# Kernel optimization log

Hardware: AMD Instinct MI355X
Metric: run time of the kernel (lower is better)

The kernel has to match this reference:

```python
import jax, jax.numpy as jnp
import numpy as np

DIM = 1024
N_HEADS = 16
HEAD_DIM = DIM // N_HEADS


def setup_inputs() -> dict:
    key = jax.random.key(0)
    ks = jax.random.split(key, 5)
    B, L = 2, 2048
    q = jax.random.normal(ks[0], (B, L, DIM), dtype=jnp.float32)
    # nn.Linear weights: shape [out_features, in_features], applied as x @ W.T
    scale = 1.0 / np.sqrt(DIM)
    Wq = jax.random.normal(ks[1], (DIM, DIM), dtype=jnp.float32) * scale
    Wk = jax.random.normal(ks[2], (DIM, DIM), dtype=jnp.float32) * scale
    Wv = jax.random.normal(ks[3], (DIM, DIM), dtype=jnp.float32) * scale
    Wo = jax.random.normal(ks[4], (DIM, DIM), dtype=jnp.float32) * scale
    return {"q": q, "Wq": Wq, "Wk": Wk, "Wv": Wv, "Wo": Wo}


def reference(q, Wq, Wk, Wv, Wo):
    B, L, _ = q.shape
    kv = q  # self-attention (kv=None path)
    # projections: x @ W.T, then split heads: b l (h d) -> b h l d
    def split_heads(x):
        return x.reshape(B, L, N_HEADS, HEAD_DIM).transpose(0, 2, 1, 3)
    qh = split_heads(q @ Wq.T)
    kh = split_heads(kv @ Wk.T)
    vh = split_heads(kv @ Wv.T)
    # scaled dot-product attention; scale = sqrt(head_dim)
    scores = jnp.einsum('bhid,bhjd->bhij', qh, kh) / jnp.sqrt(
        jnp.asarray(HEAD_DIM, dtype=qh.dtype))
    attn = jax.nn.softmax(scores, axis=-1)
    out = jnp.einsum('bhij,bhjd->bhid', attn, vh)
    # b h l d -> b l (h d)
    out = out.transpose(0, 2, 1, 3).reshape(B, L, DIM)
    return out @ Wo.T
```

## Files before the change

### kernel.cpp

```cpp
#include <hip/hip_runtime.h>


#define DIMN 1024
#define NH 16
#define HD 64
#define BB 2
#define LL 2048

typedef float f32x4 __attribute__((ext_vector_type(4)));
typedef short s16x8 __attribute__((ext_vector_type(8)));

#define QSCALE 0.18033688011112042f

static __device__ __forceinline__ unsigned short f2bf(float f) {
  unsigned u = __float_as_uint(f);
  u += 0x7fffu + ((u >> 16) & 1u);
  return (unsigned short)(u >> 16);
}
static __device__ __forceinline__ unsigned packbf2(float lo, float hi) {
  return (unsigned)f2bf(lo) | ((unsigned)f2bf(hi) << 16);
}
static __device__ __forceinline__ float xexp2(float x) {
#if __has_builtin(__builtin_amdgcn_exp2f)
  return __builtin_amdgcn_exp2f(x);
#else
  return exp2f(x);
#endif
}
static __device__ __forceinline__ s16x8 cvt8(float4 a, float4 b) {
  s16x8 r;
  r[0] = (short)f2bf(a.x); r[1] = (short)f2bf(a.y);
  r[2] = (short)f2bf(a.z); r[3] = (short)f2bf(a.w);
  r[4] = (short)f2bf(b.x); r[5] = (short)f2bf(b.y);
  r[6] = (short)f2bf(b.z); r[7] = (short)f2bf(b.w);
  return r;
}
static __device__ __forceinline__ void gld16(const unsigned short* g,
                                             unsigned short* l) {
#if __has_builtin(__builtin_amdgcn_global_load_lds)
  __builtin_amdgcn_global_load_lds(
      (const __attribute__((address_space(1))) void*)g,
      (__attribute__((address_space(3))) void*)l, 16, 0, 0);
#else
  ((uint4*)l)[threadIdx.x & 63] = ((const uint4*)g)[0];
#endif
}

__global__ __launch_bounds__(256) void cvt_all(
    const float* __restrict__ X, const float* __restrict__ Wq,
    const float* __restrict__ Wk, const float* __restrict__ Wv,
    const float* __restrict__ Wo, unsigned short* __restrict__ out) {
  const int seg = blockIdx.y;
  const float* src;
  unsigned short* dst;
  size_t n;
  if (seg == 0) { src = X; dst = out; n = (size_t)1 << 22; }
  else {
    src = (seg == 1) ? Wq : (seg == 2) ? Wk : (seg == 3) ? Wv : Wo;
    dst = out + ((size_t)1 << 22) + (size_t)(seg - 1) * (1u << 20);
    n = (size_t)1 << 20;
  }
  size_t i = ((size_t)blockIdx.x * 256 + threadIdx.x) * 8;
  if (i >= n) return;
  float4 v0 = *(const float4*)(src + i);
  float4 v1 = *(const float4*)(src + i + 4);
  uint4 o;
  o.x = packbf2(v0.x, v0.y); o.y = packbf2(v0.z, v0.w);
  o.z = packbf2(v1.x, v1.y); o.w = packbf2(v1.z, v1.w);
  *(uint4*)(dst + i) = o;
}

__global__ __launch_bounds__(256) void gemm_qkv(
    const unsigned short* __restrict__ Xb, const unsigned short* __restrict__ Wb,
    unsigned short* __restrict__ Qb, unsigned short* __restrict__ Kb,
    unsigned short* __restrict__ VT) {
  __shared__ __align__(16) unsigned short Al[128 * 32];
  __shared__ __align__(16) unsigned short Bl[128 * 32];
  const int m0 = blockIdx.x * 128;
  const int n0g = blockIdx.y * 128;
  const int sel = n0g >> 10;
  const int tid = threadIdx.x;
  const int w = tid >> 6, lane = tid & 63;
  const int c = lane & 15, quad = lane >> 4;
  const int wm = (w & 1) * 64, wn = (w >> 1) * 64;

  f32x4 zero = {0.f, 0.f, 0.f, 0.f};
  f32x4 acc[4][4];
#pragma unroll
  for (int i = 0; i < 4; ++i)
#pragma unroll
    for (int j = 0; j < 4; ++j) acc[i][j] = zero;

  const int srow = w * 32 + (lane >> 2);
  const int scol = (lane & 3) * 8;
  const unsigned short* gA = Xb + (size_t)(m0 + srow) * DIMN + scol;
  const unsigned short* gB = Wb + (size_t)(n0g + srow) * DIMN + scol;
  unsigned short* lA0 = Al + (w * 32) * 32;
  unsigned short* lA1 = Al + (w * 32 + 16) * 32;
  unsigned short* lB0 = Bl + (w * 32) * 32;
  unsigned short* lB1 = Bl + (w * 32 + 16) * 32;

  for (int k0 = 0; k0 < DIMN; k0 += 32) {
    __syncthreads();
    gld16(gA + k0, lA0);
    gld16(gA + k0 + 16 * DIMN, lA1);
    gld16(gB + k0, lB0);
    gld16(gB + k0 + 16 * DIMN, lB1);
    __syncthreads();
    s16x8 a[4], b[4];
#pragma unroll
    for (int i = 0; i < 4; ++i)
      a[i] = *(const s16x8*)&Al[(wm + i * 16 + c) * 32 + quad * 8];
#pragma unroll
    for (int j = 0; j < 4; ++j)
      b[j] = *(const s16x8*)&Bl[(wn + j * 16 + c) * 32 + quad * 8];
    if (sel != 2) {
#pragma unroll
      for (int i = 0; i < 4; ++i)
#pragma unroll
        for (int j = 0; j < 4; ++j)
          acc[i][j] = __builtin_amdgcn_mfma_f32_16x16x32_bf16(a[i], b[j], acc[i][j], 0, 0, 0);
    } else {
#pragma unroll
      for (int i = 0; i < 4; ++i)
#pragma unroll
        for (int j = 0; j < 4; ++j)
          acc[i][j] = __builtin_amdgcn_mfma_f32_16x16x32_bf16(b[j], a[i], acc[i][j], 0, 0, 0);
    }
  }

  const int n0 = n0g & 1023;
  if (sel != 2) {
    unsigned short* Out = (sel == 0) ? Qb : Kb;
    const float scale = (sel == 0) ? QSCALE : 1.0f;
#pragma unroll
    for (int i = 0; i < 4; ++i)
#pragma unroll
      for (int j = 0; j < 4; ++j)
#pragma unroll
        for (int r = 0; r < 4; ++r) {
          int row = m0 + wm + i * 16 + quad * 4 + r;
          int col = n0 + wn + j * 16 + c;
          Out[(((size_t)(row >> 11) * NH + (col >> 6)) * LL + (row & 2047)) * HD + (col & 63)] =
              f2bf(acc[i][j][r] * scale);
        }
  } else {
#pragma unroll
    for (int i = 0; i < 4; ++i)
#pragma unroll
      for (int j = 0; j < 4; ++j)
#pragma unroll
        for (int r = 0; r < 4; ++r) {
          int n = n0 + wn + j * 16 + quad * 4 + r;
          int m = m0 + wm + i * 16 + c;
          VT[(((size_t)(m >> 11) * NH + (n >> 6)) * HD + (n & 63)) * LL + (m & 2047)] =
              f2bf(acc[i][j][r]);
        }
  }
}

__global__ __launch_bounds__(256) void gemm_o(
    const unsigned short* __restrict__ A, const unsigned short* __restrict__ Wob,
    float* __restrict__ Out) {
  __shared__ __align__(16) unsigned short Al[128 * 32];
  __shared__ __align__(16) unsigned short Bl[128 * 32];
  const int m0 = blockIdx.x * 128;
  const int n0 = blockIdx.y * 128;
  const int tid = threadIdx.x;
  const int w = tid >> 6, lane = tid & 63;
  const int c = lane & 15, quad = lane >> 4;
  const int wm = (w & 1) * 64, wn = (w >> 1) * 64;

  f32x4 zero = {0.f, 0.f, 0.f, 0.f};
  f32x4 acc[4][4];
#pragma unroll
  for (int i = 0; i < 4; ++i)
#pragma unroll
    for (int j = 0; j < 4; ++j) acc[i][j] = zero;

  const int srow = w * 32 + (lane >> 2);
  const int scol = (lane & 3) * 8;
  const unsigned short* gA = A + (size_t)(m0 + srow) * DIMN + scol;
  const unsigned short* gB = Wob + (size_t)(n0 + srow) * DIMN + scol;
  unsigned short* lA0 = Al + (w * 32) * 32;
  unsigned short* lA1 = Al + (w * 32 + 16) * 32;
  unsigned short* lB0 = Bl + (w * 32) * 32;
  unsigned short* lB1 = Bl + (w * 32 + 16) * 32;

  for (int k0 = 0; k0 < DIMN; k0 += 32) {
    __syncthreads();
    gld16(gA + k0, lA0);
    gld16(gA + k0 + 16 * DIMN, lA1);
    gld16(gB + k0, lB0);
    gld16(gB + k0 + 16 * DIMN, lB1);
    __syncthreads();
    s16x8 a[4], b[4];
#pragma unroll
    for (int i = 0; i < 4; ++i)
      a[i] = *(const s16x8*)&Al[(wm + i * 16 + c) * 32 + quad * 8];
#pragma unroll
    for (int j = 0; j < 4; ++j)
      b[j] = *(const s16x8*)&Bl[(wn + j * 16 + c) * 32 + quad * 8];
#pragma unroll
    for (int i = 0; i < 4; ++i)
#pragma unroll
      for (int j = 0; j < 4; ++j)
        acc[i][j] = __builtin_amdgcn_mfma_f32_16x16x32_bf16(a[i], b[j], acc[i][j], 0, 0, 0);
  }

#pragma unroll
  for (int i = 0; i < 4; ++i)
#pragma unroll
    for (int j = 0; j < 4; ++j)
#pragma unroll
      for (int r = 0; r < 4; ++r)
        Out[(size_t)(m0 + wm + i * 16 + quad * 4 + r) * DIMN + n0 + wn + j * 16 + c] =
            acc[i][j][r];
}

__global__ __launch_bounds__(64) void qkv_proj_f(
    const float* __restrict__ X, const float* __restrict__ Wq,
    const float* __restrict__ Wk, const float* __restrict__ Wv,
    unsigned short* __restrict__ Qb, unsigned short* __restrict__ Kb,
    unsigned short* __restrict__ VT) {
  const int m0 = blockIdx.x * 64;
  const int n0g = blockIdx.y * 64;
  const int sel = n0g >> 10;
  const int n0 = n0g & 1023;
  const float* W = (sel == 0) ? Wq : (sel == 1) ? Wk : Wv;
  const int lane = threadIdx.x;
  const int c = lane & 15, quad = lane >> 4;

  f32x4 zero = {0.f, 0.f, 0.f, 0.f};
  f32x4 acc[4][4];
#pragma unroll
  for (int i = 0; i < 4; ++i)
#pragma unroll
    for (int j = 0; j < 4; ++j) acc[i][j] = zero;

  const float* ab = X + (size_t)(m0 + c) * DIMN + quad * 8;
  const float* bb = W + (size_t)(n0 + c) * DIMN + quad * 8;

  for (int k0 = 0; k0 < DIMN; k0 += 32) {
    s16x8 a[4], b[4];
#pragma unroll
    for (int i = 0; i < 4; ++i) {
      const float* p = ab + i * 16 * DIMN + k0;
      a[i] = cvt8(*(const float4*)p, *(const float4*)(p + 4));
    }
#pragma unroll
    for (int j = 0; j < 4; ++j) {
      const float* p = bb + j * 16 * DIMN + k0;
      b[j] = cvt8(*(const float4*)p, *(const float4*)(p + 4));
    }
    if (sel != 2) {
#pragma unroll
      for (int i = 0; i < 4; ++i)
#pragma unroll
        for (int j = 0; j < 4; ++j)
          acc[i][j] = __builtin_amdgcn_mfma_f32_16x16x32_bf16(a[i], b[j], acc[i][j], 0, 0, 0);
    } else {
#pragma unroll
      for (int i = 0; i < 4; ++i)
#pragma unroll
        for (int j = 0; j < 4; ++j)
          acc[i][j] = __builtin_amdgcn_mfma_f32_16x16x32_bf16(b[j], a[i], acc[i][j], 0, 0, 0);
    }
  }

  if (sel != 2) {
    unsigned short* Out = (sel == 0) ? Qb : Kb;
    const float scale = (sel == 0) ? QSCALE : 1.0f;
#pragma unroll
    for (int i = 0; i < 4; ++i)
#pragma unroll
      for (int j = 0; j < 4; ++j)
#pragma unroll
        for (int r = 0; r < 4; ++r) {
          int row = m0 + i * 16 + quad * 4 + r;
          int nl = n0 + j * 16 + c;
          int bi = row >> 11, li = row & 2047;
          int h = nl >> 6, d = nl & 63;
          Out[(((size_t)bi * NH + h) * LL + li) * HD + d] = f2bf(acc[i][j][r] * scale);
        }
  } else {
#pragma unroll
    for (int i = 0; i < 4; ++i)
#pragma unroll
      for (int j = 0; j < 4; ++j)
#pragma unroll
        for (int r = 0; r < 4; ++r) {
          int n = n0 + j * 16 + quad * 4 + r;
          int l = m0 + i * 16 + c;
          int h = n >> 6, d = n & 63;
          int bi = l >> 11, li = l & 2047;
          VT[(((size_t)bi * NH + h) * HD + d) * LL + li] = f2bf(acc[i][j][r]);
        }
  }
}

__global__ __launch_bounds__(256) void attn2(
    const unsigned short* __restrict__ Qb, const unsigned short* __restrict__ Kb,
    const unsigned short* __restrict__ VT, unsigned short* __restrict__ AO) {
  __shared__ __align__(16) unsigned short Kl[64][72];
  __shared__ __align__(16) unsigned short Vtl[64][72];
  __shared__ __align__(16) unsigned short Pl[4][16][72];

  const int bh = blockIdx.y;
  const int tid = threadIdx.x;
  const int w = tid >> 6, lane = tid & 63;
  const int c = lane & 15, quad = lane >> 4;
  const int q0 = blockIdx.x * 64 + w * 16;

  const unsigned short* Qh = Qb + (size_t)bh * LL * HD;
  const unsigned short* Kh = Kb + (size_t)bh * LL * HD;
  const unsigned short* Vh = VT + (size_t)bh * HD * LL;

  s16x8 qf0 = *(const s16x8*)(Qh + (size_t)(q0 + c) * HD + quad * 8);
  s16x8 qf1 = *(const s16x8*)(Qh + (size_t)(q0 + c) * HD + 32 + quad * 8);

  f32x4 zero = {0.f, 0.f, 0.f, 0.f};
  f32x4 o[4];
  float lsum[4] = {0.f, 0.f, 0.f, 0.f};
#pragma unroll
  for (int dc = 0; dc < 4; ++dc) o[dc] = zero;

  const int krow = tid >> 2, kq = tid & 3;
  const int vd = tid >> 2, vh = (tid >> 1) & 1, vc0 = (tid & 1) * 8;

  for (int k0 = 0; k0 < LL; k0 += 64) {
    __syncthreads();
    {
      const unsigned short* ks = Kh + (size_t)(k0 + krow) * HD + kq * 16;
      uint4 ka = *(const uint4*)ks;
      uint4 kb2 = *(const uint4*)(ks + 8);
      const unsigned short* vs = Vh + (size_t)vd * LL + k0 + vh * 32 + vc0;
      uint4 va = *(const uint4*)vs;
      uint4 vb = *(const uint4*)(vs + 16);
      *(uint4*)&Kl[krow][kq * 16] = ka;
      *(uint4*)&Kl[krow][kq * 16 + 8] = kb2;
      const unsigned* ap = (const unsigned*)&va;
      const unsigned* bp = (const unsigned*)&vb;
      unsigned ov[8];
#pragma unroll
      for (int j = 0; j < 4; ++j) {
        ov[2 * j]     = __builtin_amdgcn_perm(bp[j], ap[j], 0x05040100u);
        ov[2 * j + 1] = __builtin_amdgcn_perm(bp[j], ap[j], 0x07060302u);
      }
      uint4 w0 = {ov[0], ov[1], ov[2], ov[3]};
      uint4 w1 = {ov[4], ov[5], ov[6], ov[7]};
      *(uint4*)&Vtl[vd][vh * 32 + vc0 * 2] = w0;
      *(uint4*)&Vtl[vd][vh * 32 + vc0 * 2 + 8] = w1;
    }
    __syncthreads();

    f32x4 s[4];
#pragma unroll
    for (int t = 0; t < 4; ++t) {
      s16x8 kfa = *(const s16x8*)&Kl[t * 16 + c][quad * 8];
      s16x8 kfb = *(const s16x8*)&Kl[t * 16 + c][32 + quad * 8];
      s[t] = __builtin_amdgcn_mfma_f32_16x16x32_bf16(qf0, kfa, zero, 0, 0, 0);
      s[t] = __builtin_amdgcn_mfma_f32_16x16x32_bf16(qf1, kfb, s[t], 0, 0, 0);
    }

#pragma unroll
    for (int r = 0; r < 4; ++r) {
      float p0 = xexp2(s[0][r]);
      float p1 = xexp2(s[1][r]);
      float p2 = xexp2(s[2][r]);
      float p3 = xexp2(s[3][r]);
      lsum[r] += (p0 + p1) + (p2 + p3);
      unsigned pk01 = __builtin_amdgcn_perm(__float_as_uint(p1), __float_as_uint(p0), 0x07060302u);
      unsigned pk23 = __builtin_amdgcn_perm(__float_as_uint(p3), __float_as_uint(p2), 0x07060302u);
      int row = quad * 4 + r;
      *(unsigned*)&Pl[w][row][2 * c] = pk01;
      *(unsigned*)&Pl[w][row][32 + 2 * c] = pk23;
    }
    asm volatile("s_waitcnt lgkmcnt(0)" ::: "memory");

#pragma unroll
    for (int kk = 0; kk < 2; ++kk) {
      s16x8 pf = *(const s16x8*)&Pl[w][c][kk * 32 + quad * 8];
#pragma unroll
      for (int dc = 0; dc < 4; ++dc) {
        s16x8 vf = *(const s16x8*)&Vtl[dc * 16 + c][kk * 32 + quad * 8];
        o[dc] = __builtin_amdgcn_mfma_f32_16x16x32_bf16(pf, vf, o[dc], 0, 0, 0);
      }
    }
  }

  const int bi = bh >> 4, h = bh & 15;
#pragma unroll
  for (int r = 0; r < 4; ++r) {
    float l = lsum[r];
    l += __shfl_xor(l, 1);
    l += __shfl_xor(l, 2);
    l += __shfl_xor(l, 4);
    l += __shfl_xor(l, 8);
    float inv = 1.0f / l;
    int li = q0 + quad * 4 + r;
#pragma unroll
    for (int dc = 0; dc < 4; ++dc)
      AO[((size_t)bi * LL + li) * DIMN + h * HD + dc * 16 + c] = f2bf(o[dc][r] * inv);
  }
}

__global__ __launch_bounds__(64) void o_proj_f(
    const unsigned short* __restrict__ A, const float* __restrict__ Wo,
    float* __restrict__ Out) {
  const int m0 = blockIdx.x * 64, n0 = blockIdx.y * 64;
  const int lane = threadIdx.x;
  const int c = lane & 15, quad = lane >> 4;

  f32x4 zero = {0.f, 0.f, 0.f, 0.f};
  f32x4 acc[4][4];
#pragma unroll
  for (int i = 0; i < 4; ++i)
#pragma unroll
    for (int j = 0; j < 4; ++j) acc[i][j] = zero;

  const unsigned short* ab = A + (size_t)(m0 + c) * DIMN + quad * 8;
  const float* bb = Wo + (size_t)(n0 + c) * DIMN + quad * 8;

  for (int k0 = 0; k0 < DIMN; k0 += 32) {
    s16x8 a[4], b[4];
#pragma unroll
    for (int i = 0; i < 4; ++i) a[i] = *(const s16x8*)(ab + i * 16 * DIMN + k0);
#pragma unroll
    for (int j = 0; j < 4; ++j) {
      const float* p = bb + j * 16 * DIMN + k0;
      b[j] = cvt8(*(const float4*)p, *(const float4*)(p + 4));
    }
#pragma unroll
    for (int i = 0; i < 4; ++i)
#pragma unroll
      for (int j = 0; j < 4; ++j)
        acc[i][j] = __builtin_amdgcn_mfma_f32_16x16x32_bf16(a[i], b[j], acc[i][j], 0, 0, 0);
  }

#pragma unroll
  for (int i = 0; i < 4; ++i)
#pragma unroll
    for (int j = 0; j < 4; ++j)
#pragma unroll
      for (int r = 0; r < 4; ++r)
        Out[(size_t)(m0 + i * 16 + quad * 4 + r) * DIMN + n0 + j * 16 + c] = acc[i][j][r];
}

extern "C" void kernel_launch(void* const* d_in, const int* in_sizes, int n_in,
                              void* d_out, int out_size, void* d_ws, size_t ws_size,
                              hipStream_t stream) {
  const float* X = (const float*)d_in[0];
  const float* Wq = (const float*)d_in[1];
  const float* Wk = (const float*)d_in[2];
  const float* Wv = (const float*)d_in[3];
  const float* Wo = (const float*)d_in[4];
  float* Out = (float*)d_out;

  const size_t M1 = (size_t)1 << 20;
  unsigned short* ws16 = (unsigned short*)d_ws;

  if (ws_size >= (size_t)48 * 1024 * 1024) {
    unsigned short* Xb = ws16;
    unsigned short* Wb = ws16 + 4 * M1;
    unsigned short* Qb = ws16 + 8 * M1;
    unsigned short* Kb = ws16 + 12 * M1;
    unsigned short* VT = ws16 + 16 * M1;
    unsigned short* AO = ws16 + 20 * M1;
    cvt_all<<<dim3(2048, 5), 256, 0, stream>>>(X, Wq, Wk, Wv, Wo, ws16);
    gemm_qkv<<<dim3(32, 24), 256, 0, stream>>>(Xb, Wb, Qb, Kb, VT);
    attn2<<<dim3(LL / 64, BB * NH), 256, 0, stream>>>(Qb, Kb, VT, AO);
    gemm_o<<<dim3(32, 8), 256, 0, stream>>>(AO, Wb + 3 * M1, Out);
  } else {
    unsigned short* Qb = ws16;
    unsigned short* Kb = ws16 + 4 * M1;
    unsigned short* VT = ws16 + 8 * M1;
    unsigned short* AO = ws16 + 12 * M1;
    qkv_proj_f<<<dim3(64, 48), 64, 0, stream>>>(X, Wq, Wk, Wv, Qb, Kb, VT);
    attn2<<<dim3(LL / 64, BB * NH), 256, 0, stream>>>(Qb, Kb, VT, AO);
    o_proj_f<<<dim3(64, 16), 64, 0, stream>>>(AO, Wo, Out);
  }
}
```

Before: 210.4 us.

## Double attention query tile per wave, narrow O-proj tile, flatten conversion grid

Each attention wave now processes 32 query rows, and a block covers 128 queries. This amortizes the K/V tile loads and shared-memory staging over twice the work, at the cost of more registers and fewer blocks. The output projection uses a 128x64 tile, doubling its grid to improve CU occupancy. The bf16 conversion kernel uses a dense 1D grid, so no blocks are launched only to exit early.

Measured after the change: 201.0 us. 4.5% less time.

```diff
diff --git a/kernel.cpp b/kernel.cpp
--- a/kernel.cpp
+++ b/kernel.cpp
@@ -50,18 +50,19 @@
     const float* __restrict__ X, const float* __restrict__ Wq,
     const float* __restrict__ Wk, const float* __restrict__ Wv,
     const float* __restrict__ Wo, unsigned short* __restrict__ out) {
-  const int seg = blockIdx.y;
+  const int blk = blockIdx.x;
   const float* src;
   unsigned short* dst;
-  size_t n;
-  if (seg == 0) { src = X; dst = out; n = (size_t)1 << 22; }
-  else {
-    src = (seg == 1) ? Wq : (seg == 2) ? Wk : (seg == 3) ? Wv : Wo;
-    dst = out + ((size_t)1 << 22) + (size_t)(seg - 1) * (1u << 20);
-    n = (size_t)1 << 20;
-  }
-  size_t i = ((size_t)blockIdx.x * 256 + threadIdx.x) * 8;
-  if (i >= n) return;
+  size_t off;
+  if (blk < 2048) {
+    src = X; dst = out; off = (size_t)blk * 2048;
+  } else {
+    int s = (blk - 2048) >> 9;
+    src = (s == 0) ? Wq : (s == 1) ? Wk : (s == 2) ? Wv : Wo;
+    dst = out + ((size_t)1 << 22) + (size_t)s * (1u << 20);
+    off = (size_t)((blk - 2048) & 511) * 2048;
+  }
+  size_t i = off + (size_t)threadIdx.x * 8;
   float4 v0 = *(const float4*)(src + i);
   float4 v1 = *(const float4*)(src + i + 4);
   uint4 o;
@@ -163,167 +164,95 @@
     const unsigned short* __restrict__ A, const unsigned short* __restrict__ Wob,
     float* __restrict__ Out) {
   __shared__ __align__(16) unsigned short Al[128 * 32];
-  __shared__ __align__(16) unsigned short Bl[128 * 32];
+  __shared__ __align__(16) unsigned short Bl[64 * 32];
   const int m0 = blockIdx.x * 128;
-  const int n0 = blockIdx.y * 128;
+  const int n0 = blockIdx.y * 64;
   const int tid = threadIdx.x;
   const int w = tid >> 6, lane = tid & 63;
   const int c = lane & 15, quad = lane >> 4;
-  const int wm = (w & 1) * 64, wn = (w >> 1) * 64;
+  const int wm = (w & 1) * 64, wn = (w >> 1) * 32;
 
   f32x4 zero = {0.f, 0.f, 0.f, 0.f};
-  f32x4 acc[4][4];
+  f32x4 acc[4][2];
 #pragma unroll
   for (int i = 0; i < 4; ++i)
 #pragma unroll
-    for (int j = 0; j < 4; ++j) acc[i][j] = zero;
+    for (int j = 0; j < 2; ++j) acc[i][j] = zero;
 
   const int srow = w * 32 + (lane >> 2);
+  const int brow = w * 16 + (lane >> 2);
   const int scol = (lane & 3) * 8;
   const unsigned short* gA = A + (size_t)(m0 + srow) * DIMN + scol;
-  const unsigned short* gB = Wob + (size_t)(n0 + srow) * DIMN + scol;
+  const unsigned short* gB = Wob + (size_t)(n0 + brow) * DIMN + scol;
   unsigned short* lA0 = Al + (w * 32) * 32;
   unsigned short* lA1 = Al + (w * 32 + 16) * 32;
-  unsigned short* lB0 = Bl + (w * 32) * 32;
-  unsigned short* lB1 = Bl + (w * 32 + 16) * 32;
+  unsigned short* lB0 = Bl + (w * 16) * 32;
 
   for (int k0 = 0; k0 < DIMN; k0 += 32) {
     __syncthreads();
     gld16(gA + k0, lA0);
     gld16(gA + k0 + 16 * DIMN, lA1);
     gld16(gB + k0, lB0);
-    gld16(gB + k0 + 16 * DIMN, lB1);
     __syncthreads();
-    s16x8 a[4], b[4];
+    s16x8 a[4], b[2];
 #pragma unroll
     for (int i = 0; i < 4; ++i)
       a[i] = *(const s16x8*)&Al[(wm + i * 16 + c) * 32 + quad * 8];
 #pragma unroll
-    for (int j = 0; j < 4; ++j)
+    for (int j = 0; j < 2; ++j)
       b[j] = *(const s16x8*)&Bl[(wn + j * 16 + c) * 32 + quad * 8];
 #pragma unroll
     for (int i = 0; i < 4; ++i)
 #pragma unroll
-      for (int j = 0; j < 4; ++j)
+      for (int j = 0; j < 2; ++j)
         acc[i][j] = __builtin_amdgcn_mfma_f32_16x16x32_bf16(a[i], b[j], acc[i][j], 0, 0, 0);
   }
 
 #pragma unroll
   for (int i = 0; i < 4; ++i)
 #pragma unroll
-    for (int j = 0; j < 4; ++j)
+    for (int j = 0; j < 2; ++j)
 #pragma unroll
       for (int r = 0; r < 4; ++r)
         Out[(size_t)(m0 + wm + i * 16 + quad * 4 + r) * DIMN + n0 + wn + j * 16 + c] =
             acc[i][j][r];
 }
 
-__global__ __launch_bounds__(64) void qkv_proj_f(
-    const float* __restrict__ X, const float* __restrict__ Wq,
-    const float* __restrict__ Wk, const float* __restrict__ Wv,
-    unsigned short* __restrict__ Qb, unsigned short* __restrict__ Kb,
-    unsigned short* __restrict__ VT) {
-  const int m0 = blockIdx.x * 64;
-  const int n0g = blockIdx.y * 64;
-  const int sel = n0g >> 10;
-  const int n0 = n0g & 1023;
-  const float* W = (sel == 0) ? Wq : (sel == 1) ? Wk : Wv;
-  const int lane = threadIdx.x;
-  const int c = lane & 15, quad = lane >> 4;
-
-  f32x4 zero = {0.f, 0.f, 0.f, 0.f};
-  f32x4 acc[4][4];
-#pragma unroll
-  for (int i = 0; i < 4; ++i)
-#pragma unroll
-    for (int j = 0; j < 4; ++j) acc[i][j] = zero;
-
-  const float* ab = X + (size_t)(m0 + c) * DIMN + quad * 8;
-  const float* bb = W + (size_t)(n0 + c) * DIMN + quad * 8;
-
-  for (int k0 = 0; k0 < DIMN; k0 += 32) {
-    s16x8 a[4], b[4];
-#pragma unroll
-    for (int i = 0; i < 4; ++i) {
-      const float* p = ab + i * 16 * DIMN + k0;
-      a[i] = cvt8(*(const float4*)p, *(const float4*)(p + 4));
-    }
-#pragma unroll
-    for (int j = 0; j < 4; ++j) {
-      const float* p = bb + j * 16 * DIMN + k0;
-      b[j] = cvt8(*(const float4*)p, *(const float4*)(p + 4));
-    }
-    if (sel != 2) {
-#pragma unroll
-      for (int i = 0; i < 4; ++i)
-#pragma unroll
-        for (int j = 0; j < 4; ++j)
-          acc[i][j] = __builtin_amdgcn_mfma_f32_16x16x32_bf16(a[i], b[j], acc[i][j], 0, 0, 0);
-    } else {
-#pragma unroll
-      for (int i = 0; i < 4; ++i)
-#pragma unroll
-        for (int j = 0; j < 4; ++j)
-          acc[i][j] = __builtin_amdgcn_mfma_f32_16x16x32_bf16(b[j], a[i], acc[i][j], 0, 0, 0);
-    }
-  }
-
-  if (sel != 2) {
-    unsigned short* Out = (sel == 0) ? Qb : Kb;
-    const float scale = (sel == 0) ? QSCALE : 1.0f;
-#pragma unroll
-    for (int i = 0; i < 4; ++i)
-#pragma unroll
-      for (int j = 0; j < 4; ++j)
-#pragma unroll
-        for (int r = 0; r < 4; ++r) {
-          int row = m0 + i * 16 + quad * 4 + r;
-          int nl = n0 + j * 16 + c;
-          int bi = row >> 11, li = row & 2047;
-          int h = nl >> 6, d = nl & 63;
-          Out[(((size_t)bi * NH + h) * LL + li) * HD + d] = f2bf(acc[i][j][r] * scale);
-        }
-  } else {
-#pragma unroll
-    for (int i = 0; i < 4; ++i)
-#pragma unroll
-      for (int j = 0; j < 4; ++j)
-#pragma unroll
-        for (int r = 0; r < 4; ++r) {
-          int n = n0 + j * 16 + quad * 4 + r;
-          int l = m0 + i * 16 + c;
-          int h = n >> 6, d = n & 63;
-          int bi = l >> 11, li = l & 2047;
-          VT[(((size_t)bi * NH + h) * HD + d) * LL + li] = f2bf(acc[i][j][r]);
-        }
-  }
-}
-
-__global__ __launch_bounds__(256) void attn2(
+__global__ __launch_bounds__(256) void attn3(
     const unsigned short* __restrict__ Qb, const unsigned short* __restrict__ Kb,
     const unsigned short* __restrict__ VT, unsigned short* __restrict__ AO) {
   __shared__ __align__(16) unsigned short Kl[64][72];
   __shared__ __align__(16) unsigned short Vtl[64][72];
-  __shared__ __align__(16) unsigned short Pl[4][16][72];
+  __shared__ __align__(16) unsigned short Pl[4][32][72];
 
   const int bh = blockIdx.y;
   const int tid = threadIdx.x;
   const int w = tid >> 6, lane = tid & 63;
   const int c = lane & 15, quad = lane >> 4;
-  const int q0 = blockIdx.x * 64 + w * 16;
+  const int q0 = blockIdx.x * 128 + w * 32;
 
   const unsigned short* Qh = Qb + (size_t)bh * LL * HD;
   const unsigned short* Kh = Kb + (size_t)bh * LL * HD;
   const unsigned short* Vh = VT + (size_t)bh * HD * LL;
 
-  s16x8 qf0 = *(const s16x8*)(Qh + (size_t)(q0 + c) * HD + quad * 8);
-  s16x8 qf1 = *(const s16x8*)(Qh + (size_t)(q0 + c) * HD + 32 + quad * 8);
+  s16x8 qf[2][2];
+#pragma unroll
+  for (int m = 0; m < 2; ++m)
+#pragma unroll
+    for (int f = 0; f < 2; ++f)
+      qf[m][f] = *(const s16x8*)(Qh + (size_t)(q0 + m * 16 + c) * HD + f * 32 + quad * 8);
 
   f32x4 zero = {0.f, 0.f, 0.f, 0.f};
-  f32x4 o[4];
-  float lsum[4] = {0.f, 0.f, 0.f, 0.f};
-#pragma unroll
-  for (int dc = 0; dc < 4; ++dc) o[dc] = zero;
+  f32x4 o[2][4];
+  float lsum[2][4];
+#pragma unroll
+  for (int m = 0; m < 2; ++m)
+#pragma unroll
+    for (int r = 0; r < 4; ++r) lsum[m][r] = 0.f;
+#pragma unroll
+  for (int m = 0; m < 2; ++m)
+#pragma unroll
+    for (int dc = 0; dc < 4; ++dc) o[m][dc] = zero;
 
   const int krow = tid >> 2, kq = tid & 3;
   const int vd = tid >> 2, vh = (tid >> 1) & 1, vc0 = (tid & 1) * 8;
@@ -354,54 +283,144 @@
     }
     __syncthreads();
 
-    f32x4 s[4];
+    f32x4 s[2][4];
 #pragma unroll
     for (int t = 0; t < 4; ++t) {
       s16x8 kfa = *(const s16x8*)&Kl[t * 16 + c][quad * 8];
       s16x8 kfb = *(const s16x8*)&Kl[t * 16 + c][32 + quad * 8];
-      s[t] = __builtin_amdgcn_mfma_f32_16x16x32_bf16(qf0, kfa, zero, 0, 0, 0);
-      s[t] = __builtin_amdgcn_mfma_f32_16x16x32_bf16(qf1, kfb, s[t], 0, 0, 0);
-    }
-
-#pragma unroll
-    for (int r = 0; r < 4; ++r) {
-      float p0 = xexp2(s[0][r]);
-      float p1 = xexp2(s[1][r]);
-      float p2 = xexp2(s[2][r]);
-      float p3 = xexp2(s[3][r]);
-      lsum[r] += (p0 + p1) + (p2 + p3);
-      unsigned pk01 = __builtin_amdgcn_perm(__float_as_uint(p1), __float_as_uint(p0), 0x07060302u);
-      unsigned pk23 = __builtin_amdgcn_perm(__float_as_uint(p3), __float_as_uint(p2), 0x07060302u);
-      int row = quad * 4 + r;
-      *(unsigned*)&Pl[w][row][2 * c] = pk01;
-      *(unsigned*)&Pl[w][row][32 + 2 * c] = pk23;
-    }
+#pragma unroll
+      for (int m = 0; m < 2; ++m) {
+        s[m][t] = __builtin_amdgcn_mfma_f32_16x16x32_bf16(qf[m][0], kfa, zero, 0, 0, 0);
+        s[m][t] = __builtin_amdgcn_mfma_f32_16x16x32_bf16(qf[m][1], kfb, s[m][t], 0, 0, 0);
+      }
+    }
+
+#pragma unroll
+    for (int m = 0; m < 2; ++m)
+#pragma unroll
+      for (int r = 0; r < 4; ++r) {
+        float p0 = xexp2(s[m][0][r]);
+        float p1 = xexp2(s[m][1][r]);
+        float p2 = xexp2(s[m][2][r]);
+        float p3 = xexp2(s[m][3][r]);
+        lsum[m][r] += (p0 + p1) + (p2 + p3);
+        unsigned pk01 = __builtin_amdgcn_perm(__float_as_uint(p1), __float_as_uint(p0), 0x07060302u);
+        unsigned pk23 = __builtin_amdgcn_perm(__float_as_uint(p3), __float_as_uint(p2), 0x07060302u);
+        int row = m * 16 + quad * 4 + r;
+        *(unsigned*)&Pl[w][row][2 * c] = pk01;
+        *(unsigned*)&Pl[w][row][32 + 2 * c] = pk23;
+      }
     asm volatile("s_waitcnt lgkmcnt(0)" ::: "memory");
 
 #pragma unroll
     for (int kk = 0; kk < 2; ++kk) {
-      s16x8 pf = *(const s16x8*)&Pl[w][c][kk * 32 + quad * 8];
+      s16x8 pf0 = *(const s16x8*)&Pl[w][c][kk * 32 + quad * 8];
+      s16x8 pf1 = *(const s16x8*)&Pl[w][16 + c][kk * 32 + quad * 8];
 #pragma unroll
       for (int dc = 0; dc < 4; ++dc) {
         s16x8 vf = *(const s16x8*)&Vtl[dc * 16 + c][kk * 32 + quad * 8];
-        o[dc] = __builtin_amdgcn_mfma_f32_16x16x32_bf16(pf, vf, o[dc], 0, 0, 0);
+        o[0][dc] = __builtin_amdgcn_mfma_f32_16x16x32_bf16(pf0, vf, o[0][dc], 0, 0, 0);
+        o[1][dc] = __builtin_amdgcn_mfma_f32_16x16x32_bf16(pf1, vf, o[1][dc], 0, 0, 0);
       }
     }
   }
 
   const int bi = bh >> 4, h = bh & 15;
 #pragma unroll
-  for (int r = 0; r < 4; ++r) {
-    float l = lsum[r];
-    l += __shfl_xor(l, 1);
-    l += __shfl_xor(l, 2);
-    l += __shfl_xor(l, 4);
-    l += __shfl_xor(l, 8);
-    float inv = 1.0f / l;
-    int li = q0 + quad * 4 + r;
-#pragma unroll
-    for (int dc = 0; dc < 4; ++dc)
-      AO[((size_t)bi * LL + li) * DIMN + h * HD + dc * 16 + c] = f2bf(o[dc][r] * inv);
+  for (int m = 0; m < 2; ++m)
+#pragma unroll
+    for (int r = 0; r < 4; ++r) {
+      float l = lsum[m][r];
+      l += __shfl_xor(l, 1);
+      l += __shfl_xor(l, 2);
+      l += __shfl_xor(l, 4);
+      l += __shfl_xor(l, 8);
+      float inv = 1.0f / l;
+      int li = q0 + m * 16 + quad * 4 + r;
+#pragma unroll
+      for (int dc = 0; dc < 4; ++dc)
+        AO[((size_t)bi * LL + li) * DIMN + h * HD + dc * 16 + c] = f2bf(o[m][dc][r] * inv);
+    }
+}
+
+__global__ __launch_bounds__(64) void qkv_proj_f(
+    const float* __restrict__ X, const float* __restrict__ Wq,
+    const float* __restrict__ Wk, const float* __restrict__ Wv,
+    unsigned short* __restrict__ Qb, unsigned short* __restrict__ Kb,
+    unsigned short* __restrict__ VT) {
+  const int m0 = blockIdx.x * 64;
+  const int n0g = blockIdx.y * 64;
+  const int sel = n0g >> 10;
+  const int n0 = n0g & 1023;
+  const float* W = (sel == 0) ? Wq : (sel == 1) ? Wk : Wv;
+  const int lane = threadIdx.x;
+  const int c = lane & 15, quad = lane >> 4;
+
+  f32x4 zero = {0.f, 0.f, 0.f, 0.f};
+  f32x4 acc[4][4];
+#pragma unroll
+  for (int i = 0; i < 4; ++i)
+#pragma unroll
+    for (int j = 0; j < 4; ++j) acc[i][j] = zero;
+
+  const float* ab = X + (size_t)(m0 + c) * DIMN + quad * 8;
+  const float* bb = W + (size_t)(n0 + c) * DIMN + quad * 8;
+
+  for (int k0 = 0; k0 < DIMN; k0 += 32) {
+    s16x8 a[4], b[4];
+#pragma unroll
+    for (int i = 0; i < 4; ++i) {
+      const float* p = ab + i * 16 * DIMN + k0;
+      a[i] = cvt8(*(const float4*)p, *(const float4*)(p + 4));
+    }
+#pragma unroll
+    for (int j = 0; j < 4; ++j) {
+      const float* p = bb + j * 16 * DIMN + k0;
+      b[j] = cvt8(*(const float4*)p, *(const float4*)(p + 4));
+    }
+    if (sel != 2) {
+#pragma unroll
+      for (int i = 0; i < 4; ++i)
+#pragma unroll
+        for (int j = 0; j < 4; ++j)
+          acc[i][j] = __builtin_amdgcn_mfma_f32_16x16x32_bf16(a[i], b[j], acc[i][j], 0, 0, 0);
+    } else {
+#pragma unroll
+      for (int i = 0; i < 4; ++i)
+#pragma unroll
+        for (int j = 0; j < 4; ++j)
+          acc[i][j] = __builtin_amdgcn_mfma_f32_16x16x32_bf16(b[j], a[i], acc[i][j], 0, 0, 0);
+    }
+  }
+
+  if (sel != 2) {
+    unsigned short* Out = (sel == 0) ? Qb : Kb;
+    const float scale = (sel == 0) ? QSCALE : 1.0f;
+#pragma unroll
+    for (int i = 0; i < 4; ++i)
+#pragma unroll
+      for (int j = 0; j < 4; ++j)
+#pragma unroll
+        for (int r = 0; r < 4; ++r) {
+          int row = m0 + i * 16 + quad * 4 + r;
+          int nl = n0 + j * 16 + c;
+          int bi = row >> 11, li = row & 2047;
+          int h = nl >> 6, d = nl & 63;
+          Out[(((size_t)bi * NH + h) * LL + li) * HD + d] = f2bf(acc[i][j][r] * scale);
+        }
+  } else {
+#pragma unroll
+    for (int i = 0; i < 4; ++i)
+#pragma unroll
+      for (int j = 0; j < 4; ++j)
+#pragma unroll
+        for (int r = 0; r < 4; ++r) {
+          int n = n0 + j * 16 + quad * 4 + r;
+          int l = m0 + i * 16 + c;
+          int h = n >> 6, d = n & 63;
+          int bi = l >> 11, li = l & 2047;
+          VT[(((size_t)bi * NH + h) * HD + d) * LL + li] = f2bf(acc[i][j][r]);
+        }
   }
 }
 
@@ -467,17 +486,17 @@
     unsigned short* Kb = ws16 + 12 * M1;
     unsigned short* VT = ws16 + 16 * M1;
     unsigned short* AO = ws16 + 20 * M1;
-    cvt_all<<<dim3(2048, 5), 256, 0, stream>>>(X, Wq, Wk, Wv, Wo, ws16);
+    cvt_all<<<4096, 256, 0, stream>>>(X, Wq, Wk, Wv, Wo, ws16);
     gemm_qkv<<<dim3(32, 24), 256, 0, stream>>>(Xb, Wb, Qb, Kb, VT);
-    attn2<<<dim3(LL / 64, BB * NH), 256, 0, stream>>>(Qb, Kb, VT, AO);
-    gemm_o<<<dim3(32, 8), 256, 0, stream>>>(AO, Wb + 3 * M1, Out);
+    attn3<<<dim3(LL / 128, BB * NH), 256, 0, stream>>>(Qb, Kb, VT, AO);
+    gemm_o<<<dim3(32, 16), 256, 0, stream>>>(AO, Wb + 3 * M1, Out);
   } else {
     unsigned short* Qb = ws16;
     unsigned short* Kb = ws16 + 4 * M1;
     unsigned short* VT = ws16 + 8 * M1;
     unsigned short* AO = ws16 + 12 * M1;
     qkv_proj_f<<<dim3(64, 48), 64, 0, stream>>>(X, Wq, Wk, Wv, Qb, Kb, VT);
-    attn2<<<dim3(LL / 64, BB * NH), 256, 0, stream>>>(Qb, Kb, VT, AO);
+    attn3<<<dim3(LL / 128, BB * NH), 256, 0, stream>>>(Qb, Kb, VT, AO);
     o_proj_f<<<dim3(64, 16), 64, 0, stream>>>(AO, Wo, Out);
   }
 }
```
